# Optimization experiments

Measured on AMD Instinct MI355X. Metric: run time of the kernel, lower is better.

The kernel has to match this reference:

```python
import jax, jax.numpy as jnp
import numpy as np

B, N, INPUT_DIM = 32, 4096, 256
BASE = 32           # base_feat_dim
A = 5               # n_aggs
E = 48              # per_agg_dim
H = 2               # num_agg_heads
HD = E // H         # head dim = 24
AGG_DIM = BASE * A  # 160
HIDDEN = 512
EXTRA_IN = INPUT_DIM - AGG_DIM   # 96
EXTRA_OUT = HIDDEN - E * A       # 272


def setup_inputs() -> dict:
    key = jax.random.key(0)
    ks = jax.random.split(key, 10)
    s = 0.05
    return {
        "x": jax.random.normal(ks[0], (B, N, INPUT_DIM), dtype=jnp.float32),
        # 5 per-group Linear(base_feat_dim -> 48), stacked: [A, E, BASE]
        "agg_W": jax.random.normal(ks[1], (A, E, BASE), dtype=jnp.float32) * s,
        "agg_b": jax.random.normal(ks[2], (A, E), dtype=jnp.float32) * s,
        # MultiheadAttention packed in-projection [3E, E] and bias [3E]
        "in_proj_w": jax.random.normal(ks[3], (3 * E, E), dtype=jnp.float32) * s,
        "in_proj_b": jax.random.normal(ks[4], (3 * E,), dtype=jnp.float32) * s,
        "out_w": jax.random.normal(ks[5], (E, E), dtype=jnp.float32) * s,
        "out_b": jax.random.normal(ks[6], (E,), dtype=jnp.float32) * s,
        # extra Linear(96 -> 272)
        "extra_w": jax.random.normal(ks[7], (EXTRA_OUT, EXTRA_IN), dtype=jnp.float32) * s,
        "extra_b": jax.random.normal(ks[8], (EXTRA_OUT,), dtype=jnp.float32) * s,
    }


def reference(x, agg_W, agg_b, in_proj_w, in_proj_b, out_w, out_b, extra_w, extra_b):
    b, n, _ = x.shape
    agg_feat = x[..., :AGG_DIM].reshape(b, n, A, BASE)      # [B,N,A,BASE]
    extra_feat = x[..., AGG_DIM:]                            # [B,N,EXTRA_IN]

    # fused per-group projections (one batched GEMM)
    proj = jnp.einsum("bnad,aed->bnae", agg_feat, agg_W) + agg_b  # [B,N,A,E]

    # faithful to torch: stack(dim=1) -> [B,A,N,E], then reshape(B*N, A, E)
    stacked = jnp.transpose(proj, (0, 2, 1, 3)).reshape(b * n, A, E)

    # MultiheadAttention (eval mode; attn dropout inactive)
    qkv = stacked @ in_proj_w.T + in_proj_b                  # [M,A,3E]
    q, k, v = jnp.split(qkv, 3, axis=-1)
    def heads(t):  # [M,A,E] -> [M,H,A,HD]
        return t.reshape(-1, A, H, HD).transpose(0, 2, 1, 3)
    q, k, v = heads(q), heads(k), heads(v)
    scores = jnp.einsum("mhqd,mhkd->mhqk", q, k) / np.sqrt(HD).astype(np.float32)
    attn = jax.nn.softmax(scores, axis=-1)
    o = jnp.einsum("mhqk,mhkd->mhqd", attn, v)               # [M,H,A,HD]
    o = o.transpose(0, 2, 1, 3).reshape(-1, A, E)            # [M,A,E]
    attn_out = o @ out_w.T + out_b

    agg_out = attn_out.reshape(b, n, A * E)                  # [B,N,240]
    extra_out = extra_feat @ extra_w.T + extra_b             # [B,N,272]
    return jnp.concatenate([agg_out, extra_out], axis=-1)    # [B,N,512]
```

## Files before the change

kernel.cpp:

```cpp
#include <hip/hip_runtime.h>

#define NTOK (32*4096)
#define WQ_FLOATS (5*144*32)

__global__ void setup_wqkv(const float* __restrict__ aggW,
                           const float* __restrict__ aggB,
                           const float* __restrict__ ipw,
                           const float* __restrict__ ipb,
                           float* __restrict__ Wq,
                           float* __restrict__ bq)
{
    int t = blockIdx.x*256 + threadIdx.x;
    if (t >= 5*144) return;
    int a = t / 144;
    int r = t - a*144;
    float scale = (r < 48) ? 0.20412414523193154f : 1.0f;
    const float* wrow = ipw + r*48;
    float bacc = ipb[r];
    for (int e = 0; e < 48; ++e) bacc += wrow[e]*aggB[a*48 + e];
    bq[t] = bacc*scale;
    for (int d = 0; d < 32; ++d) {
        float acc = 0.f;
        for (int e = 0; e < 48; ++e) acc += wrow[e]*aggW[(a*48 + e)*32 + d];
        Wq[t*32 + d] = acc*scale;
    }
}

__device__ __forceinline__ void load_xchunk(const float* __restrict__ p, float xr[32])
{
    const float4* xv = reinterpret_cast<const float4*>(p);
#pragma unroll
    for (int i = 0; i < 8; ++i) {
        float4 t = xv[i];
        xr[4*i+0] = t.x; xr[4*i+1] = t.y; xr[4*i+2] = t.z; xr[4*i+3] = t.w;
    }
}

__device__ __forceinline__ float row32(const float* __restrict__ wrow, const float xr[32], float bias)
{
    const float4* wp = reinterpret_cast<const float4*>(wrow);
    float a0 = bias, a1 = 0.f, a2 = 0.f, a3 = 0.f;
#pragma unroll
    for (int i = 0; i < 2; ++i) {
        float4 w4 = wp[i];
        a0 = fmaf(w4.x, xr[4*i+0], a0); a0 = fmaf(w4.y, xr[4*i+1], a0);
        a0 = fmaf(w4.z, xr[4*i+2], a0); a0 = fmaf(w4.w, xr[4*i+3], a0);
    }
#pragma unroll
    for (int i = 2; i < 4; ++i) {
        float4 w4 = wp[i];
        a1 = fmaf(w4.x, xr[4*i+0], a1); a1 = fmaf(w4.y, xr[4*i+1], a1);
        a1 = fmaf(w4.z, xr[4*i+2], a1); a1 = fmaf(w4.w, xr[4*i+3], a1);
    }
#pragma unroll
    for (int i = 4; i < 6; ++i) {
        float4 w4 = wp[i];
        a2 = fmaf(w4.x, xr[4*i+0], a2); a2 = fmaf(w4.y, xr[4*i+1], a2);
        a2 = fmaf(w4.z, xr[4*i+2], a2); a2 = fmaf(w4.w, xr[4*i+3], a2);
    }
#pragma unroll
    for (int i = 6; i < 8; ++i) {
        float4 w4 = wp[i];
        a3 = fmaf(w4.x, xr[4*i+0], a3); a3 = fmaf(w4.y, xr[4*i+1], a3);
        a3 = fmaf(w4.z, xr[4*i+2], a3); a3 = fmaf(w4.w, xr[4*i+3], a3);
    }
    return (a0 + a1) + (a2 + a3);
}

__global__ __launch_bounds__(256) void attn_main(
    const float* __restrict__ x,
    const float* __restrict__ Wq,
    const float* __restrict__ bq,
    const float* __restrict__ outw,
    const float* __restrict__ outb,
    float* __restrict__ out)
{
    __shared__ float sAll[11856];
    float* sW   = sAll;
    float* sB   = sAll + 9216;
    float* sOWT = sAll + 9504;
    float* sOB  = sAll + 11808;

    const int t = (int)threadIdx.x;
    const unsigned g0 = blockIdx.x * 240u;
    const unsigned u0 = g0 >> 12;
    const unsigned a0 = u0 - 5u*((u0*52429u) >> 18);
    const unsigned a1 = (a0 == 4u) ? 0u : a0 + 1u;

    {
        const float4* s0p = reinterpret_cast<const float4*>(Wq + a0*4608u);
        const float4* s1p = reinterpret_cast<const float4*>(Wq + a1*4608u);
        float4* d0 = reinterpret_cast<float4*>(sW);
        float4* d1 = reinterpret_cast<float4*>(sW + 4608);
#pragma unroll
        for (int i = 0; i < 5; ++i) {
            int idx = t + 256*i;
            if (idx < 1152) { d0[idx] = s0p[idx]; d1[idx] = s1p[idx]; }
        }
#pragma unroll
        for (int i = 0; i < 9; ++i) {
            int idx = t + 256*i;
            int f = idx / 48, j = idx - f*48;
            sOWT[idx] = outw[j*48 + f];
        }
        if (t < 144) { sB[t] = bq[a0*144u + t]; sB[144 + t] = bq[a1*144u + t]; }
        if (t >= 192 && t < 240) sOB[t - 192] = outb[t - 192];
    }
    __syncthreads();

    const int lane = t & 63;
    if (lane >= 60) return;
    const int wv = t >> 6;
    const unsigned m_base = (blockIdx.x*4u + (unsigned)wv)*12u;
    const unsigned tok5 = (unsigned)lane / 5u;
    const unsigned aq   = (unsigned)lane - tok5*5u;
    const unsigned m = m_base + tok5;
    if (m >= NTOK) return;

    const unsigned g  = 5u*m_base + (unsigned)lane;
    const unsigned u  = g >> 12;
    const unsigned bb = (u*52429u) >> 18;
    const unsigned a  = u - 5u*bb;
    const float* xp = x + ((((bb<<12) | (g & 4095u)) << 8) + (a<<5));

    const int sel = (a == a0) ? 0 : 1;
    const float* myW = sW + sel*4608;
    const float* myB = sB + sel*144;

    float xr[32]; load_xchunk(xp, xr);

    const int base4 = (lane - (int)aq)*4;
    int ad[4];
#pragma unroll
    for (int r = 0; r < 4; ++r) {
        int sl = (int)aq + r + 1; if (sl >= 5) sl -= 5;
        ad[r] = base4 + sl*4;
    }

    float s0[5] = {0,0,0,0,0}, s1[5] = {0,0,0,0,0};
#pragma unroll 1
    for (int e = 0; e < 24; ++e) {
        float qe = row32(myW + e*32, xr, myB[e]);
        float ke = row32(myW + (48+e)*32, xr, myB[48+e]);
        s0[0] = fmaf(qe, ke, s0[0]);
#pragma unroll
        for (int r = 0; r < 4; ++r) {
            float kr = __int_as_float(__builtin_amdgcn_ds_bpermute(ad[r], __float_as_int(ke)));
            s0[r+1] = fmaf(qe, kr, s0[r+1]);
        }
    }
#pragma unroll 1
    for (int e = 24; e < 48; ++e) {
        float qe = row32(myW + e*32, xr, myB[e]);
        float ke = row32(myW + (48+e)*32, xr, myB[48+e]);
        s1[0] = fmaf(qe, ke, s1[0]);
#pragma unroll
        for (int r = 0; r < 4; ++r) {
            float kr = __int_as_float(__builtin_amdgcn_ds_bpermute(ad[r], __float_as_int(ke)));
            s1[r+1] = fmaf(qe, kr, s1[r+1]);
        }
    }

    float p0[5], p1[5];
    {
        float mx = fmaxf(fmaxf(fmaxf(s0[0], s0[1]), fmaxf(s0[2], s0[3])), s0[4]);
        float e0 = __expf(s0[0]-mx), e1 = __expf(s0[1]-mx), e2 = __expf(s0[2]-mx),
              e3 = __expf(s0[3]-mx), e4 = __expf(s0[4]-mx);
        float inv = 1.0f/(e0+e1+e2+e3+e4);
        p0[0]=e0*inv; p0[1]=e1*inv; p0[2]=e2*inv; p0[3]=e3*inv; p0[4]=e4*inv;
    }
    {
        float mx = fmaxf(fmaxf(fmaxf(s1[0], s1[1]), fmaxf(s1[2], s1[3])), s1[4]);
        float e0 = __expf(s1[0]-mx), e1 = __expf(s1[1]-mx), e2 = __expf(s1[2]-mx),
              e3 = __expf(s1[3]-mx), e4 = __expf(s1[4]-mx);
        float inv = 1.0f/(e0+e1+e2+e3+e4);
        p1[0]=e0*inv; p1[1]=e1*inv; p1[2]=e2*inv; p1[3]=e3*inv; p1[4]=e4*inv;
    }

    float oj[48];
    {
        const float4* b4 = reinterpret_cast<const float4*>(sOB);
#pragma unroll
        for (int j4 = 0; j4 < 12; ++j4) {
            float4 v = b4[j4];
            oj[4*j4+0]=v.x; oj[4*j4+1]=v.y; oj[4*j4+2]=v.z; oj[4*j4+3]=v.w;
        }
    }
#pragma unroll 1
    for (int e = 0; e < 24; ++e) {
        float ve = row32(myW + (96+e)*32, xr, myB[96+e]);
        float oe = p0[0]*ve;
#pragma unroll
        for (int r = 0; r < 4; ++r) {
            float vr = __int_as_float(__builtin_amdgcn_ds_bpermute(ad[r], __float_as_int(ve)));
            oe = fmaf(p0[r+1], vr, oe);
        }
        const float4* owr = reinterpret_cast<const float4*>(sOWT + e*48);
#pragma unroll
        for (int j4 = 0; j4 < 12; ++j4) {
            float4 w4 = owr[j4];
            oj[4*j4+0] = fmaf(w4.x, oe, oj[4*j4+0]);
            oj[4*j4+1] = fmaf(w4.y, oe, oj[4*j4+1]);
            oj[4*j4+2] = fmaf(w4.z, oe, oj[4*j4+2]);
            oj[4*j4+3] = fmaf(w4.w, oe, oj[4*j4+3]);
        }
    }
#pragma unroll 1
    for (int e = 24; e < 48; ++e) {
        float ve = row32(myW + (96+e)*32, xr, myB[96+e]);
        float oe = p1[0]*ve;
#pragma unroll
        for (int r = 0; r < 4; ++r) {
            float vr = __int_as_float(__builtin_amdgcn_ds_bpermute(ad[r], __float_as_int(ve)));
            oe = fmaf(p1[r+1], vr, oe);
        }
        const float4* owr = reinterpret_cast<const float4*>(sOWT + e*48);
#pragma unroll
        for (int j4 = 0; j4 < 12; ++j4) {
            float4 w4 = owr[j4];
            oj[4*j4+0] = fmaf(w4.x, oe, oj[4*j4+0]);
            oj[4*j4+1] = fmaf(w4.y, oe, oj[4*j4+1]);
            oj[4*j4+2] = fmaf(w4.z, oe, oj[4*j4+2]);
            oj[4*j4+3] = fmaf(w4.w, oe, oj[4*j4+3]);
        }
    }

    float4* d4 = reinterpret_cast<float4*>(out + (size_t)m*512u + aq*48u);
#pragma unroll
    for (int j4 = 0; j4 < 12; ++j4)
        d4[j4] = make_float4(oj[4*j4+0], oj[4*j4+1], oj[4*j4+2], oj[4*j4+3]);
}

__global__ __launch_bounds__(256) void extra_gemm(
    const float* __restrict__ x,
    const float* __restrict__ exw,
    const float* __restrict__ exb,
    float* __restrict__ out)
{
    __shared__ float sw[34*96*4];

    const int t = (int)threadIdx.x;
    const unsigned tb = blockIdx.x >> 1;
    const int half = (int)(blockIdx.x & 1u);
    const int colbase = half*136;

#pragma unroll 1
    for (int q = t; q < 3264; q += 256) {
        int row = q / 24;
        int kp  = (q - row*24)*4;
        float4 v = *reinterpret_cast<const float4*>(
            exw + (size_t)(colbase + row)*96u + (unsigned)kp);
        int c4 = row >> 2, jp = row & 3;
        float* dp = sw + (c4*96 + kp)*4 + jp;
        dp[0] = v.x; dp[4] = v.y; dp[8] = v.z; dp[12] = v.w;
    }

    const unsigned m = tb*256u + (unsigned)t;
    float xr[96];
    {
        const float4* xp = reinterpret_cast<const float4*>(x + (size_t)m*256u + 160u);
#pragma unroll
        for (int i = 0; i < 24; ++i) {
            float4 v = xp[i];
            xr[4*i+0]=v.x; xr[4*i+1]=v.y; xr[4*i+2]=v.z; xr[4*i+3]=v.w;
        }
    }
    __syncthreads();

    float* __restrict__ dst = out + (size_t)m*512u + 240u + (unsigned)colbase;
    const float4* bp = reinterpret_cast<const float4*>(exb + colbase);
#pragma unroll 1
    for (int c4 = 0; c4 < 34; ++c4) {
        const float4* wp = reinterpret_cast<const float4*>(sw + c4*384);
        float4 acc = bp[c4];
#pragma unroll
        for (int k = 0; k < 96; ++k) {
            float4 w4 = wp[k];
            acc.x = fmaf(w4.x, xr[k], acc.x);
            acc.y = fmaf(w4.y, xr[k], acc.y);
            acc.z = fmaf(w4.z, xr[k], acc.z);
            acc.w = fmaf(w4.w, xr[k], acc.w);
        }
        reinterpret_cast<float4*>(dst)[c4] = acc;
    }
}

extern "C" void kernel_launch(void* const* d_in, const int* in_sizes, int n_in,
                              void* d_out, int out_size, void* d_ws, size_t ws_size,
                              hipStream_t stream)
{
    const float* x    = (const float*)d_in[0];
    const float* aggW = (const float*)d_in[1];
    const float* aggB = (const float*)d_in[2];
    const float* ipw  = (const float*)d_in[3];
    const float* ipb  = (const float*)d_in[4];
    const float* outw = (const float*)d_in[5];
    const float* outb = (const float*)d_in[6];
    const float* exw  = (const float*)d_in[7];
    const float* exb  = (const float*)d_in[8];
    float* out = (float*)d_out;

    float* Wq = (float*)d_ws;
    float* bq = Wq + WQ_FLOATS;

    setup_wqkv<<<dim3(3), dim3(256), 0, stream>>>(aggW, aggB, ipw, ipb, Wq, bq);
    attn_main<<<dim3((NTOK + 47)/48), dim3(256), 0, stream>>>(x, Wq, bq, outw, outb, out);
    extra_gemm<<<dim3(512*2), dim3(256), 0, stream>>>(x, exw, exb, out);
}
```

Measured before the change: 741.2 us.

## Fold out-projection into V weights and split straddling attention blocks

The setup kernel now folds the MHA out-projection into per-head V weights and biases, precomputed per aggregation group. The main kernel therefore computes 96 V-like rows and mixes them with attention probabilities, with no per-token 48x48 out-projection and fewer registers. Blocks whose rows span two aggregation groups move to a separate straddle kernel, so the common kernel loads only one weight set into shared memory and can run at higher occupancy. The extra GEMM is split into quarters instead of halves to use less shared memory, at the cost of more weight staging and an extra launch.

```diff
diff --git a/kernel.cpp b/kernel.cpp
--- a/kernel.cpp
+++ b/kernel.cpp
@@ -1,28 +1,72 @@
 #include <hip/hip_runtime.h>
 
 #define NTOK (32*4096)
-#define WQ_FLOATS (5*144*32)
-
-__global__ void setup_wqkv(const float* __restrict__ aggW,
-                           const float* __restrict__ aggB,
-                           const float* __restrict__ ipw,
-                           const float* __restrict__ ipb,
-                           float* __restrict__ Wq,
-                           float* __restrict__ bq)
-{
-    int t = blockIdx.x*256 + threadIdx.x;
-    if (t >= 5*144) return;
-    int a = t / 144;
-    int r = t - a*144;
-    float scale = (r < 48) ? 0.20412414523193154f : 1.0f;
-    const float* wrow = ipw + r*48;
-    float bacc = ipb[r];
-    for (int e = 0; e < 48; ++e) bacc += wrow[e]*aggB[a*48 + e];
-    bq[t] = bacc*scale;
-    for (int d = 0; d < 32; ++d) {
+#define NROWS (NTOK*5)
+#define WF_STRIDE 6144
+#define BF_STRIDE 192
+
+__global__ __launch_bounds__(256) void setup_fused(
+    const float* __restrict__ aggW,
+    const float* __restrict__ aggB,
+    const float* __restrict__ ipw,
+    const float* __restrict__ ipb,
+    const float* __restrict__ outw,
+    const float* __restrict__ outb,
+    float* __restrict__ Wf,
+    float* __restrict__ bf)
+{
+    const int a = (int)blockIdx.x;
+    const int t = (int)threadIdx.x;
+    __shared__ float wv[1536];
+    __shared__ float bv[48];
+
+    for (int idx = t; idx < 1536; idx += 256) {
+        int f = idx >> 5, d = idx & 31;
         float acc = 0.f;
-        for (int e = 0; e < 48; ++e) acc += wrow[e]*aggW[(a*48 + e)*32 + d];
-        Wq[t*32 + d] = acc*scale;
+        for (int e = 0; e < 48; ++e)
+            acc += ipw[(96+f)*48 + e] * aggW[(a*48 + e)*32 + d];
+        wv[idx] = acc;
+    }
+    if (t < 48) {
+        float acc = ipb[96 + t];
+        for (int e = 0; e < 48; ++e)
+            acc += ipw[(96+t)*48 + e] * aggB[a*48 + e];
+        bv[t] = acc;
+    }
+    __syncthreads();
+
+    const float qs = 0.20412414523193154f;
+    for (int idx = t; idx < 3072; idx += 256) {
+        int r = idx >> 5, d = idx & 31;
+        float acc = 0.f;
+        for (int e = 0; e < 48; ++e)
+            acc += ipw[r*48 + e] * aggW[(a*48 + e)*32 + d];
+        if (r < 48) acc *= qs;
+        Wf[a*WF_STRIDE + idx] = acc;
+    }
+    for (int idx = t; idx < 3072; idx += 256) {
+        int rr = idx >> 5, d = idx & 31;
+        int j  = (rr < 48) ? rr : rr - 48;
+        int fb = (rr < 48) ? 0 : 24;
+        float acc = 0.f;
+        for (int ff = 0; ff < 24; ++ff)
+            acc += outw[j*48 + fb + ff] * wv[(fb + ff)*32 + d];
+        Wf[a*WF_STRIDE + 3072 + idx] = acc;
+    }
+    if (t < 96) {
+        float acc = ipb[t];
+        for (int e = 0; e < 48; ++e)
+            acc += ipw[t*48 + e] * aggB[a*48 + e];
+        if (t < 48) acc *= qs;
+        bf[a*BF_STRIDE + t] = acc;
+    } else if (t < 192) {
+        int rr = t - 96;
+        int j  = (rr < 48) ? rr : rr - 48;
+        int fb = (rr < 48) ? 0 : 24;
+        float acc = (rr < 48) ? outb[j] : 0.f;
+        for (int ff = 0; ff < 24; ++ff)
+            acc += outw[j*48 + fb + ff] * bv[fb + ff];
+        bf[a*BF_STRIDE + t] = acc;
     }
 }
 
@@ -67,51 +111,38 @@
     return (a0 + a1) + (a2 + a3);
 }
 
-__global__ __launch_bounds__(256) void attn_main(
-    const float* __restrict__ x,
-    const float* __restrict__ Wq,
-    const float* __restrict__ bq,
-    const float* __restrict__ outw,
-    const float* __restrict__ outb,
-    float* __restrict__ out)
-{
-    __shared__ float sAll[11856];
-    float* sW   = sAll;
-    float* sB   = sAll + 9216;
-    float* sOWT = sAll + 9504;
-    float* sOB  = sAll + 11808;
-
+template<int NSETS>
+__device__ __forceinline__ void attn_body(
+    int blk, const float* __restrict__ x,
+    const float* __restrict__ Wf, const float* __restrict__ bf,
+    float* __restrict__ out, float* sW, float* sB)
+{
     const int t = (int)threadIdx.x;
-    const unsigned g0 = blockIdx.x * 240u;
+    const unsigned g0 = (unsigned)blk * 240u;
     const unsigned u0 = g0 >> 12;
     const unsigned a0 = u0 - 5u*((u0*52429u) >> 18);
-    const unsigned a1 = (a0 == 4u) ? 0u : a0 + 1u;
 
     {
-        const float4* s0p = reinterpret_cast<const float4*>(Wq + a0*4608u);
-        const float4* s1p = reinterpret_cast<const float4*>(Wq + a1*4608u);
+        const float4* s0p = reinterpret_cast<const float4*>(Wf + a0*WF_STRIDE);
         float4* d0 = reinterpret_cast<float4*>(sW);
-        float4* d1 = reinterpret_cast<float4*>(sW + 4608);
-#pragma unroll
-        for (int i = 0; i < 5; ++i) {
-            int idx = t + 256*i;
-            if (idx < 1152) { d0[idx] = s0p[idx]; d1[idx] = s1p[idx]; }
-        }
-#pragma unroll
-        for (int i = 0; i < 9; ++i) {
-            int idx = t + 256*i;
-            int f = idx / 48, j = idx - f*48;
-            sOWT[idx] = outw[j*48 + f];
-        }
-        if (t < 144) { sB[t] = bq[a0*144u + t]; sB[144 + t] = bq[a1*144u + t]; }
-        if (t >= 192 && t < 240) sOB[t - 192] = outb[t - 192];
+#pragma unroll
+        for (int i = 0; i < 6; ++i) d0[t + 256*i] = s0p[t + 256*i];
+        if (t < BF_STRIDE) sB[t] = bf[a0*BF_STRIDE + t];
+        if (NSETS == 2) {
+            const unsigned a1 = (a0 == 4u) ? 0u : a0 + 1u;
+            const float4* s1p = reinterpret_cast<const float4*>(Wf + a1*WF_STRIDE);
+            float4* d1 = reinterpret_cast<float4*>(sW + WF_STRIDE);
+#pragma unroll
+            for (int i = 0; i < 6; ++i) d1[t + 256*i] = s1p[t + 256*i];
+            if (t < BF_STRIDE) sB[BF_STRIDE + t] = bf[a1*BF_STRIDE + t];
+        }
     }
     __syncthreads();
 
     const int lane = t & 63;
     if (lane >= 60) return;
-    const int wv = t >> 6;
-    const unsigned m_base = (blockIdx.x*4u + (unsigned)wv)*12u;
+    const int wv_ = t >> 6;
+    const unsigned m_base = ((unsigned)blk*4u + (unsigned)wv_)*12u;
     const unsigned tok5 = (unsigned)lane / 5u;
     const unsigned aq   = (unsigned)lane - tok5*5u;
     const unsigned m = m_base + tok5;
@@ -123,9 +154,14 @@
     const unsigned a  = u - 5u*bb;
     const float* xp = x + ((((bb<<12) | (g & 4095u)) << 8) + (a<<5));
 
-    const int sel = (a == a0) ? 0 : 1;
-    const float* myW = sW + sel*4608;
-    const float* myB = sB + sel*144;
+    const float* myW;
+    const float* myB;
+    if (NSETS == 1) { myW = sW; myB = sB; }
+    else {
+        const int sel = (a == a0) ? 0 : 1;
+        myW = sW + sel*WF_STRIDE;
+        myB = sB + sel*BF_STRIDE;
+    }
 
     float xr[32]; load_xchunk(xp, xr);
 
@@ -177,81 +213,79 @@
         p1[0]=e0*inv; p1[1]=e1*inv; p1[2]=e2*inv; p1[3]=e3*inv; p1[4]=e4*inv;
     }
 
-    float oj[48];
-    {
-        const float4* b4 = reinterpret_cast<const float4*>(sOB);
-#pragma unroll
-        for (int j4 = 0; j4 < 12; ++j4) {
-            float4 v = b4[j4];
-            oj[4*j4+0]=v.x; oj[4*j4+1]=v.y; oj[4*j4+2]=v.z; oj[4*j4+3]=v.w;
-        }
-    }
-#pragma unroll 1
-    for (int e = 0; e < 24; ++e) {
-        float ve = row32(myW + (96+e)*32, xr, myB[96+e]);
-        float oe = p0[0]*ve;
-#pragma unroll
-        for (int r = 0; r < 4; ++r) {
-            float vr = __int_as_float(__builtin_amdgcn_ds_bpermute(ad[r], __float_as_int(ve)));
-            oe = fmaf(p0[r+1], vr, oe);
-        }
-        const float4* owr = reinterpret_cast<const float4*>(sOWT + e*48);
-#pragma unroll
-        for (int j4 = 0; j4 < 12; ++j4) {
-            float4 w4 = owr[j4];
-            oj[4*j4+0] = fmaf(w4.x, oe, oj[4*j4+0]);
-            oj[4*j4+1] = fmaf(w4.y, oe, oj[4*j4+1]);
-            oj[4*j4+2] = fmaf(w4.z, oe, oj[4*j4+2]);
-            oj[4*j4+3] = fmaf(w4.w, oe, oj[4*j4+3]);
-        }
-    }
-#pragma unroll 1
-    for (int e = 24; e < 48; ++e) {
-        float ve = row32(myW + (96+e)*32, xr, myB[96+e]);
-        float oe = p1[0]*ve;
-#pragma unroll
-        for (int r = 0; r < 4; ++r) {
-            float vr = __int_as_float(__builtin_amdgcn_ds_bpermute(ad[r], __float_as_int(ve)));
-            oe = fmaf(p1[r+1], vr, oe);
-        }
-        const float4* owr = reinterpret_cast<const float4*>(sOWT + e*48);
-#pragma unroll
-        for (int j4 = 0; j4 < 12; ++j4) {
-            float4 w4 = owr[j4];
-            oj[4*j4+0] = fmaf(w4.x, oe, oj[4*j4+0]);
-            oj[4*j4+1] = fmaf(w4.y, oe, oj[4*j4+1]);
-            oj[4*j4+2] = fmaf(w4.z, oe, oj[4*j4+2]);
-            oj[4*j4+3] = fmaf(w4.w, oe, oj[4*j4+3]);
-        }
-    }
-
-    float4* d4 = reinterpret_cast<float4*>(out + (size_t)m*512u + aq*48u);
-#pragma unroll
-    for (int j4 = 0; j4 < 12; ++j4)
-        d4[j4] = make_float4(oj[4*j4+0], oj[4*j4+1], oj[4*j4+2], oj[4*j4+3]);
-}
-
-__global__ __launch_bounds__(256) void extra_gemm(
+    float* __restrict__ dst = out + (size_t)m*512u + aq*48u;
+#pragma unroll 1
+    for (int eg = 0; eg < 6; ++eg) {
+        float oj[8];
+#pragma unroll
+        for (int e2 = 0; e2 < 8; ++e2) {
+            const int e = eg*8 + e2;
+            float vA = row32(myW + (96+e)*32,  xr, myB[96+e]);
+            float vB = row32(myW + (144+e)*32, xr, myB[144+e]);
+            float oe = p0[0]*vA + p1[0]*vB;
+#pragma unroll
+            for (int r = 0; r < 4; ++r) {
+                float vAr = __int_as_float(__builtin_amdgcn_ds_bpermute(ad[r], __float_as_int(vA)));
+                float vBr = __int_as_float(__builtin_amdgcn_ds_bpermute(ad[r], __float_as_int(vB)));
+                oe = fmaf(p0[r+1], vAr, oe);
+                oe = fmaf(p1[r+1], vBr, oe);
+            }
+            oj[e2] = oe;
+        }
+        float4* d4 = reinterpret_cast<float4*>(dst + eg*8);
+        d4[0] = make_float4(oj[0], oj[1], oj[2], oj[3]);
+        d4[1] = make_float4(oj[4], oj[5], oj[6], oj[7]);
+    }
+}
+
+__global__ __launch_bounds__(256, 5) void attn_main(
+    const float* __restrict__ x, const float* __restrict__ Wf,
+    const float* __restrict__ bf, float* __restrict__ out)
+{
+    __shared__ float sW[WF_STRIDE];
+    __shared__ float sB[BF_STRIDE];
+    const int blk = (int)blockIdx.x;
+    const unsigned g0 = (unsigned)blk*240u;
+    unsigned gend = g0 + 239u; if (gend > NROWS-1u) gend = NROWS-1u;
+    if ((g0 >> 12) != (gend >> 12)) return;
+    attn_body<1>(blk, x, Wf, bf, out, sW, sB);
+}
+
+__global__ __launch_bounds__(256) void attn_straddle(
+    const float* __restrict__ x, const float* __restrict__ Wf,
+    const float* __restrict__ bf, float* __restrict__ out)
+{
+    __shared__ float sW[2*WF_STRIDE];
+    __shared__ float sB[2*BF_STRIDE];
+    const int bi = (int)blockIdx.x + 1;
+    const int blk = (bi << 12) / 240;
+    const unsigned g0 = (unsigned)blk*240u;
+    unsigned gend = g0 + 239u; if (gend > NROWS-1u) gend = NROWS-1u;
+    if ((g0 >> 12) == (gend >> 12)) return;
+    attn_body<2>(blk, x, Wf, bf, out, sW, sB);
+}
+
+__global__ __launch_bounds__(256, 4) void extra_gemm(
     const float* __restrict__ x,
     const float* __restrict__ exw,
     const float* __restrict__ exb,
     float* __restrict__ out)
 {
-    __shared__ float sw[34*96*4];
+    __shared__ float sw2[17*96*4];
 
     const int t = (int)threadIdx.x;
-    const unsigned tb = blockIdx.x >> 1;
-    const int half = (int)(blockIdx.x & 1u);
-    const int colbase = half*136;
-
-#pragma unroll 1
-    for (int q = t; q < 3264; q += 256) {
+    const unsigned tb = blockIdx.x >> 2;
+    const int quarter = (int)(blockIdx.x & 3u);
+    const int colbase = quarter*68;
+
+#pragma unroll 1
+    for (int q = t; q < 1632; q += 256) {
         int row = q / 24;
         int kp  = (q - row*24)*4;
         float4 v = *reinterpret_cast<const float4*>(
             exw + (size_t)(colbase + row)*96u + (unsigned)kp);
         int c4 = row >> 2, jp = row & 3;
-        float* dp = sw + (c4*96 + kp)*4 + jp;
+        float* dp = sw2 + (c4*96 + kp)*4 + jp;
         dp[0] = v.x; dp[4] = v.y; dp[8] = v.z; dp[12] = v.w;
     }
 
@@ -268,11 +302,11 @@
     __syncthreads();
 
     float* __restrict__ dst = out + (size_t)m*512u + 240u + (unsigned)colbase;
-    const float4* bp = reinterpret_cast<const float4*>(exb + colbase);
-#pragma unroll 1
-    for (int c4 = 0; c4 < 34; ++c4) {
-        const float4* wp = reinterpret_cast<const float4*>(sw + c4*384);
-        float4 acc = bp[c4];
+    const float* bp = exb + colbase;
+#pragma unroll 1
+    for (int c4 = 0; c4 < 17; ++c4) {
+        const float4* wp = reinterpret_cast<const float4*>(sw2 + c4*384);
+        float4 acc = make_float4(bp[c4*4+0], bp[c4*4+1], bp[c4*4+2], bp[c4*4+3]);
 #pragma unroll
         for (int k = 0; k < 96; ++k) {
             float4 w4 = wp[k];
@@ -300,10 +334,11 @@
     const float* exb  = (const float*)d_in[8];
     float* out = (float*)d_out;
 
-    float* Wq = (float*)d_ws;
-    float* bq = Wq + WQ_FLOATS;
-
-    setup_wqkv<<<dim3(3), dim3(256), 0, stream>>>(aggW, aggB, ipw, ipb, Wq, bq);
-    attn_main<<<dim3((NTOK + 47)/48), dim3(256), 0, stream>>>(x, Wq, bq, outw, outb, out);
-    extra_gemm<<<dim3(512*2), dim3(256), 0, stream>>>(x, exw, exb, out);
-}
+    float* Wf = (float*)d_ws;
+    float* bf = Wf + 5*WF_STRIDE;
+
+    setup_fused<<<dim3(5), dim3(256), 0, stream>>>(aggW, aggB, ipw, ipb, outw, outb, Wf, bf);
+    attn_main<<<dim3((NROWS + 239)/240), dim3(256), 0, stream>>>(x, Wf, bf, out);
+    attn_straddle<<<dim3(159), dim3(256), 0, stream>>>(x, Wf, bf, out);
+    extra_gemm<<<dim3((NTOK/256)*4), dim3(256), 0, stream>>>(x, exw, exb, out);
+}
```

Result: slower. 2.031 ms (+174.0%).
